# Performance work log

Measured on AMD Instinct MI355X. Metric: run time of the kernel, lower is better.

Reference implementation:

```python
import jax, jax.numpy as jnp
import numpy as np

B, N, D, F, H, C, L = 64, 8192, 5, 16, 4, 4, 4
NEG_SLOPE = 0.2


def setup_inputs() -> dict:
    key = jax.random.key(0)
    ks = jax.random.split(key, 16)
    lin = lambda k, fi, fo: (jax.random.normal(k, (fi, fo), jnp.float32) / np.sqrt(fi)).astype(jnp.float32)
    x = jax.random.normal(ks[0], (B, N, F), jnp.float32)
    agent_nodes = jax.random.randint(ks[1], (B,), 0, N, dtype=jnp.int32)
    neighbors = jax.random.randint(ks[2], (N, D), 0, N, dtype=jnp.int32)
    # GATv2 params (L layers, all 16 -> 4 heads x 4 = 16)
    Wl = jax.random.normal(ks[3], (L, F, H, C), jnp.float32) / np.sqrt(F)
    Wr = jax.random.normal(ks[4], (L, F, H, C), jnp.float32) / np.sqrt(F)
    att_w = jax.random.normal(ks[5], (L, H, C), jnp.float32) / np.sqrt(C)
    bias = jnp.zeros((L, H * C), jnp.float32)
    # global classifier 16->32->64, edge classifier 99->16->8->1
    Wg1, bg1 = lin(ks[6], H * C, 2 * H * C), jnp.zeros(2 * H * C, jnp.float32)
    Wg2, bg2 = lin(ks[7], 2 * H * C, 4 * H * C), jnp.zeros(4 * H * C, jnp.float32)
    e_in = 2 * H * C + 3 + 4 * H * C  # 99
    We1, be1 = lin(ks[8], e_in, H * C), jnp.zeros(H * C, jnp.float32)
    We2, be2 = lin(ks[9], H * C, H * C // 2), jnp.zeros(H * C // 2, jnp.float32)
    We3, be3 = lin(ks[10], H * C // 2, 1), jnp.zeros(1, jnp.float32)
    return dict(x=x, agent_nodes=agent_nodes, neighbors=neighbors, Wl=Wl, Wr=Wr,
                att_w=att_w, bias=bias, Wg1=Wg1, bg1=bg1, Wg2=Wg2, bg2=bg2,
                We1=We1, be1=be1, We2=We2, be2=be2, We3=We3, be3=be3)


def _gatv2_layer(h, src, dst, wl, wr, a, b, n_nodes):
    # h: [B,N,Fin]; wl/wr: [Fin,H,C]; a: [H,C]; b: [H*C]
    xl = jnp.einsum('bnf,fhc->bnhc', h, wl)   # source transform
    xr = jnp.einsum('bnf,fhc->bnhc', h, wr)   # target transform
    hs = xl[:, src]                            # [B,E,H,C]
    ht = xr[:, dst]
    logit = jnp.einsum('behc,hc->beh', jax.nn.leaky_relu(hs + ht, NEG_SLOPE), a)
    lt = logit.transpose(1, 0, 2)              # [E,B,H] (segment ops need E first)
    m = jax.ops.segment_max(lt, dst, num_segments=n_nodes)
    w = jnp.exp(lt - m[dst])
    s = jax.ops.segment_sum(w, dst, num_segments=n_nodes)
    alpha = w / (s[dst] + 1e-16)               # [E,B,H] softmax over in-edges of dst
    msg = alpha[..., None] * hs.transpose(1, 0, 2, 3)
    out = jax.ops.segment_sum(msg, dst, num_segments=n_nodes)  # [N,B,H,C]
    return out.transpose(1, 0, 2, 3).reshape(h.shape[0], n_nodes, -1) + b


def reference(x, agent_nodes, neighbors, Wl, Wr, att_w, bias,
              Wg1, bg1, Wg2, bg2, We1, be1, We2, be2, We3, be3):
    Bn, Nn, _ = x.shape
    Dd = neighbors.shape[1]
    loop = jnp.arange(Nn, dtype=neighbors.dtype)
    src = jnp.concatenate([jnp.repeat(loop, Dd), loop])   # add_self_loops
    dst = jnp.concatenate([neighbors.reshape(-1), loop])
    h = x
    for i in range(Wl.shape[0]):
        h = _gatv2_layer(h, src, dst, Wl[i], Wr[i], att_w[i], bias[i], Nn)
    # global mean aggregation -> 2 SlimFC(tanh)
    agg = jnp.tanh(h.mean(axis=1) @ Wg1 + bg1)
    agg = jnp.tanh(agg @ Wg2 + bg2)                        # [B,64]
    # agent out-edges: source node + its D neighbors
    nb = neighbors[agent_nodes]                            # [B,D]
    bi = jnp.arange(Bn)
    source = h[bi, agent_nodes]                            # [B,16]
    target = h[bi[:, None], nb]                            # [B,D,16]
    tok = jnp.eye(3, dtype=h.dtype)                        # 3 one-hot act tokens
    feats = jnp.concatenate([
        jnp.broadcast_to(source[:, None, None, :], (Bn, 3, Dd, source.shape[-1])),
        jnp.broadcast_to(tok[None, :, None, :], (Bn, 3, Dd, 3)),
        jnp.broadcast_to(target[:, None, :, :], (Bn, 3, Dd, target.shape[-1])),
        jnp.broadcast_to(agg[:, None, None, :], (Bn, 3, Dd, agg.shape[-1])),
    ], axis=-1)                                            # [B,3,D,99]
    e = jnp.tanh(feats @ We1 + be1)
    e = jnp.tanh(e @ We2 + be2)
    e = (e @ We3 + be3)[..., 0]                            # [B,3,D]
    # logits[b, turn*D + move] (convert_multidiscrete_action_to_discrete)
    return e.reshape(Bn, 3 * Dd)
```

## Files before the change

kernel.cpp:

```cpp
#include <hip/hip_runtime.h>
#include <hip/hip_fp16.h>
#include <cmath>

#define NNODES 8192
#define NB 64
#define ND 5
#define MAXDEG 64
#define NBLK_L 2048



__global__ void __launch_bounds__(1024)
k_init(const int* __restrict__ agent, const int* __restrict__ nbr,
       int* __restrict__ cnt, int* __restrict__ slot, int* __restrict__ needed) {
  int t = threadIdx.x;
  for (int v = t; v < NNODES; v += 1024) {
    cnt[v] = 1;
    slot[v*MAXDEG] = v;
    needed[v] = 0;
  }
  __syncthreads();
  if (t < NB) {
    int an = agent[t];
    needed[an] = 1;
    #pragma unroll
    for (int d = 0; d < ND; ++d) needed[nbr[an*ND + d]] = 1;
  }
}


__global__ void __launch_bounds__(256)
k_t0fill(const float* __restrict__ x, const float* __restrict__ Wl0, const float* __restrict__ Wr0,
         __half* __restrict__ xl0, __half* __restrict__ xr0,
         const int* __restrict__ nbr, int* __restrict__ cnt, int* __restrict__ slot) {
  if (blockIdx.x >= NBLK_L) {
    int i = (blockIdx.x - NBLK_L)*256 + threadIdx.x;
    if (i < NNODES*ND) {
      int v = nbr[i];
      int pos = atomicAdd(&cnt[v], 1);
      slot[v*MAXDEG + pos] = i/ND;
    }
    return;
  }
  int gid = blockIdx.x*blockDim.x + threadIdx.x;
  int n = gid >> 6;
  int b = gid & 63;
  const float4* src = (const float4*)(x + (((size_t)b*NNODES + n) << 4));
  float hv[16];
  #pragma unroll
  for (int q = 0; q < 4; ++q) *(float4*)(hv+4*q) = src[q];
  float yl[16], yr[16];
  #pragma unroll
  for (int j = 0; j < 16; ++j) { yl[j] = 0.f; yr[j] = 0.f; }
  #pragma unroll
  for (int f = 0; f < 16; ++f) {
    float hf = hv[f];
    #pragma unroll
    for (int j = 0; j < 16; ++j) {
      yl[j] = fmaf(hf, Wl0[f*16+j], yl[j]);
      yr[j] = fmaf(hf, Wr0[f*16+j], yr[j]);
    }
  }
  size_t idx = ((size_t)n << 10) + (b << 4);
  __half2 lh[8], rh[8];
  #pragma unroll
  for (int j = 0; j < 8; ++j) {
    lh[j] = __floats2half2_rn(yl[2*j], yl[2*j+1]);
    rh[j] = __floats2half2_rn(yr[2*j], yr[2*j+1]);
  }
  float4* ld = (float4*)(xl0 + idx);
  ld[0] = *(float4*)&lh[0]; ld[1] = *(float4*)&lh[4];
  float4* rd = (float4*)(xr0 + idx);
  rd[0] = *(float4*)&rh[0]; rd[1] = *(float4*)&rh[4];
}


template<bool LAST>
__global__ void __launch_bounds__(256)
k_layer(const __half* __restrict__ xlin, const __half* __restrict__ xrin,
        __half* __restrict__ xlout, __half* __restrict__ xrout,
        const float* __restrict__ WlNext, const float* __restrict__ WrNext,
        const float* __restrict__ att, const float* __restrict__ bias,
        const int* __restrict__ cnt, const int* __restrict__ slot,
        const int* __restrict__ needed, __half* __restrict__ h,
        float* __restrict__ meanpart) {
  __shared__ float msm[4096];
  int gid = blockIdx.x*blockDim.x + threadIdx.x;
  int v = gid >> 6;
  int b = gid & 63;
  int w = threadIdx.x >> 6;
  size_t boff = (size_t)(b << 4);

  float xr[16];
  {
    const float4* rp = (const float4*)(xrin + ((size_t)v << 10) + boff);
    float4 r0 = rp[0], r1 = rp[1];
    const __half2* pa = (const __half2*)&r0;
    const __half2* pb = (const __half2*)&r1;
    #pragma unroll
    for (int q = 0; q < 4; ++q) { float2 f = __half22float2(pa[q]); xr[2*q] = f.x; xr[2*q+1] = f.y; }
    #pragma unroll
    for (int q = 0; q < 4; ++q) { float2 f = __half22float2(pb[q]); xr[8+2*q] = f.x; xr[8+2*q+1] = f.y; }
  }
  float aw[16];
  #pragma unroll
  for (int j = 0; j < 16; ++j) aw[j] = att[j];

  float s4[4] = {0.f, 0.f, 0.f, 0.f};
  float acc[16];
  #pragma unroll
  for (int j = 0; j < 16; ++j) acc[j] = 0.f;

  int deg = cnt[v];
  const int* sl = slot + v*MAXDEG;

  auto loadrow = [&](int u, float4& r0, float4& r1) {
    const float4* sp = (const float4*)(xlin + ((size_t)u << 10) + boff);
    r0 = sp[0]; r1 = sp[1];
  };
  auto process = [&](const float4& r0, const float4& r1) {
    float t[16];
    const __half2* pa = (const __half2*)&r0;
    const __half2* pb = (const __half2*)&r1;
    #pragma unroll
    for (int q = 0; q < 4; ++q) { float2 f = __half22float2(pa[q]); t[2*q] = f.x; t[2*q+1] = f.y; }
    #pragma unroll
    for (int q = 0; q < 4; ++q) { float2 f = __half22float2(pb[q]); t[8+2*q] = f.x; t[8+2*q+1] = f.y; }
    #pragma unroll
    for (int hh = 0; hh < 4; ++hh) {
      float lg = 0.f;
      #pragma unroll
      for (int c = 0; c < 4; ++c) {
        float z = t[hh*4+c] + xr[hh*4+c];
        z = (z >= 0.f) ? z : 0.2f*z;
        lg = fmaf(z, aw[hh*4+c], lg);
      }
      float p = __expf(lg);
      s4[hh] += p;
      #pragma unroll
      for (int c = 0; c < 4; ++c) acc[hh*4+c] = fmaf(p, t[hh*4+c], acc[hh*4+c]);
    }
  };

  float4 r00,r01, r10,r11, r20,r21, r30,r31, r40,r41, r50,r51, p0,p1;
  loadrow(sl[0], r00, r01);
  if (deg > 1) loadrow(sl[1], r10, r11);
  if (deg > 2) loadrow(sl[2], r20, r21);
  if (deg > 3) loadrow(sl[3], r30, r31);
  if (deg > 4) loadrow(sl[4], r40, r41);
  if (deg > 5) loadrow(sl[5], r50, r51);
  if (deg > 6) loadrow(sl[6], p0, p1);
  process(r00, r01);
  if (deg > 1) process(r10, r11);
  if (deg > 2) process(r20, r21);
  if (deg > 3) process(r30, r31);
  if (deg > 4) process(r40, r41);
  if (deg > 5) process(r50, r51);
  for (int e = 6; e < deg; ++e) {
    float4 c0 = p0, c1 = p1;
    if (e+1 < deg) loadrow(sl[e+1], p0, p1);
    process(c0, c1);
  }

  float o[16];
  #pragma unroll
  for (int hh = 0; hh < 4; ++hh) {
    float inv = 1.f / s4[hh];
    #pragma unroll
    for (int c = 0; c < 4; ++c) o[hh*4+c] = fmaf(acc[hh*4+c], inv, bias[hh*4+c]);
  }

  if (!LAST) {
    float yl[16], yr[16];
    #pragma unroll
    for (int j = 0; j < 16; ++j) { yl[j] = 0.f; yr[j] = 0.f; }
    #pragma unroll
    for (int f = 0; f < 16; ++f) {
      float of = o[f];
      #pragma unroll
      for (int j = 0; j < 16; ++j) {
        yl[j] = fmaf(of, WlNext[f*16+j], yl[j]);
        yr[j] = fmaf(of, WrNext[f*16+j], yr[j]);
      }
    }
    __half2 lh[8], rh[8];
    #pragma unroll
    for (int j = 0; j < 8; ++j) {
      lh[j] = __floats2half2_rn(yl[2*j], yl[2*j+1]);
      rh[j] = __floats2half2_rn(yr[2*j], yr[2*j+1]);
    }
    size_t idx = ((size_t)v << 10) + boff;
    float4* ld = (float4*)(xlout + idx);
    ld[0] = *(float4*)&lh[0]; ld[1] = *(float4*)&lh[4];
    float4* rd = (float4*)(xrout + idx);
    rd[0] = *(float4*)&rh[0]; rd[1] = *(float4*)&rh[4];
  } else {
    if (needed[v]) {
      __half2 oh[8];
      #pragma unroll
      for (int j = 0; j < 8; ++j) oh[j] = __floats2half2_rn(o[2*j], o[2*j+1]);
      float4* hd = (float4*)(h + ((size_t)v << 10) + boff);
      hd[0] = *(float4*)&oh[0]; hd[1] = *(float4*)&oh[4];
    }
    #pragma unroll
    for (int j = 0; j < 16; ++j) msm[(w << 10) + (b << 4) + j] = o[j];
    __syncthreads();
    for (int i = threadIdx.x; i < 1024; i += 256) {
      float s = msm[i] + msm[1024+i] + msm[2048+i] + msm[3072+i];
      meanpart[(size_t)blockIdx.x*1024 + i] = s;
    }
  }
}


__global__ void __launch_bounds__(256)
k_tail(const __half* __restrict__ h, const int* __restrict__ agent,
       const int* __restrict__ nbr, const float* __restrict__ meanpart,
       const float* __restrict__ Wg1, const float* __restrict__ bg1,
       const float* __restrict__ Wg2, const float* __restrict__ bg2,
       const float* __restrict__ We1, const float* __restrict__ be1,
       const float* __restrict__ We2, const float* __restrict__ be2,
       const float* __restrict__ We3, const float* __restrict__ be3,
       float* __restrict__ out) {
  int b = blockIdx.x;
  int t = threadIdx.x;
  __shared__ float red[256];
  __shared__ float mean[16], g1[32], aggs[64];
  __shared__ float srcv[16];
  __shared__ float tgt[5][16];
  __shared__ float e1s[15][16];
  __shared__ float e2s[15][8];
  int an = agent[b];

  {
    int hc = t & 15, grp = t >> 4;
    float s = 0.f;
    for (int p = grp*128; p < grp*128+128; ++p) s += meanpart[(size_t)p*1024 + b*16 + hc];
    red[t] = s;
    __syncthreads();
    if (t < 16) {
      float m = 0.f;
      for (int g = 0; g < 16; ++g) m += red[g*16 + t];
      mean[t] = m * (1.0f/NNODES);
    }
  }
  if (t >= 64 && t < 80) srcv[t-64] = __half2float(h[((size_t)an << 10) + (b << 4) + (t-64)]);
  if (t >= 96 && t < 176) {
    int d = (t-96)/16, k = (t-96)%16;
    int nn = nbr[an*ND + d];
    tgt[d][k] = __half2float(h[((size_t)nn << 10) + (b << 4) + k]);
  }
  __syncthreads();
  if (t < 32) {
    float a = bg1[t];
    for (int f = 0; f < 16; ++f) a = fmaf(mean[f], Wg1[f*32+t], a);
    g1[t] = tanhf(a);
  }
  __syncthreads();
  if (t < 64) {
    float a = bg2[t];
    for (int f = 0; f < 32; ++f) a = fmaf(g1[f], Wg2[f*64+t], a);
    aggs[t] = tanhf(a);
  }
  __syncthreads();
  if (t < 240) {
    int j = t & 15, td = t >> 4;
    int tk = td/5, d = td%5;
    float a = be1[j];
    for (int k = 0; k < 16; ++k) a = fmaf(srcv[k],  We1[k*16+j],      a);
    a += We1[(16+tk)*16 + j];
    for (int k = 0; k < 16; ++k) a = fmaf(tgt[d][k], We1[(19+k)*16+j], a);
    for (int k = 0; k < 64; ++k) a = fmaf(aggs[k],  We1[(35+k)*16+j], a);
    e1s[td][j] = tanhf(a);
  }
  __syncthreads();
  if (t < 120) {
    int j = t & 7, td = t >> 3;
    float a = be2[j];
    for (int k = 0; k < 16; ++k) a = fmaf(e1s[td][k], We2[k*8+j], a);
    e2s[td][j] = tanhf(a);
  }
  __syncthreads();
  if (t < 15) {
    float a = be3[0];
    for (int k = 0; k < 8; ++k) a = fmaf(e2s[t][k], We3[k], a);
    out[b*15 + t] = a;
  }
}


extern "C" void kernel_launch(void* const* d_in, const int* in_sizes, int n_in,
                              void* d_out, int out_size, void* d_ws, size_t ws_size,
                              hipStream_t stream) {
  const float* x     = (const float*)d_in[0];
  const int*   agent = (const int*)  d_in[1];
  const int*   nbr   = (const int*)  d_in[2];
  const float* Wl    = (const float*)d_in[3];
  const float* Wr    = (const float*)d_in[4];
  const float* att   = (const float*)d_in[5];
  const float* bias  = (const float*)d_in[6];
  const float* Wg1   = (const float*)d_in[7];
  const float* bg1   = (const float*)d_in[8];
  const float* Wg2   = (const float*)d_in[9];
  const float* bg2   = (const float*)d_in[10];
  const float* We1   = (const float*)d_in[11];
  const float* be1   = (const float*)d_in[12];
  const float* We2   = (const float*)d_in[13];
  const float* be2   = (const float*)d_in[14];
  const float* We3   = (const float*)d_in[15];
  const float* be3   = (const float*)d_in[16];
  float* out = (float*)d_out;

  char* ws = (char*)d_ws;
  size_t off = 0;
  auto alloc = [&](size_t bytes) -> void* {
    void* p = ws + off;
    off += (bytes + 255) & ~(size_t)255;
    return p;
  };
  const size_t XBYTES  = (size_t)NNODES*NB*16*sizeof(__half);
  __half* h    = (__half*)alloc(XBYTES);
  __half* xlA  = (__half*)alloc(XBYTES);
  __half* xlB  = (__half*)alloc(XBYTES);
  __half* xrA  = (__half*)alloc(XBYTES);
  __half* xrB  = (__half*)alloc(XBYTES);
  int* cnt     = (int*)alloc(NNODES*sizeof(int));
  int* needed  = (int*)alloc(NNODES*sizeof(int));
  int* slot    = (int*)alloc((size_t)NNODES*MAXDEG*sizeof(int));
  float* meanpart = (float*)alloc((size_t)NBLK_L*1024*sizeof(float));

  k_init<<<1, 1024, 0, stream>>>(agent, nbr, cnt, slot, needed);
  k_t0fill<<<NBLK_L + NNODES*ND/256, 256, 0, stream>>>(x, Wl, Wr, xlA, xrA, nbr, cnt, slot);

  k_layer<false><<<NBLK_L, 256, 0, stream>>>(xlA, xrA, xlB, xrB, Wl + 256, Wr + 256,
                                             att,      bias,      cnt, slot, needed, nullptr, nullptr);
  k_layer<false><<<NBLK_L, 256, 0, stream>>>(xlB, xrB, xlA, xrA, Wl + 512, Wr + 512,
                                             att + 16, bias + 16, cnt, slot, needed, nullptr, nullptr);
  k_layer<false><<<NBLK_L, 256, 0, stream>>>(xlA, xrA, xlB, xrB, Wl + 768, Wr + 768,
                                             att + 32, bias + 32, cnt, slot, needed, nullptr, nullptr);
  k_layer<true ><<<NBLK_L, 256, 0, stream>>>(xlB, xrB, nullptr, nullptr, nullptr, nullptr,
                                             att + 48, bias + 48, cnt, slot, needed, h, meanpart);

  k_tail<<<NB, 256, 0, stream>>>(h, agent, nbr, meanpart,
                                 Wg1, bg1, Wg2, bg2,
                                 We1, be1, We2, be2, We3, be3, out);
}
```

Measured before the change: 245.9 us.

## Split each node-batch across two wavefronts and replace init kernel with memset

Each node's 16-channel feature vector per batch element is now split across two wavefronts (8 channels each), so every lane does one 16-byte gather per neighbor instead of two. The two halves are exchanged through shared memory before the next-layer projection. The layer grid doubles to 4096 blocks, which raises parallelism and memory-level concurrency but adds a __syncthreads and doubles the partial-mean buffer that k_tail must reduce. The separate single-block init kernel is replaced by a memset plus extra blocks in the fill kernel, and the self-loop is handled implicitly rather than stored in the slot table.

Result: slower. 305.4 us (+24.2%).

```diff
diff --git a/kernel.cpp b/kernel.cpp
--- a/kernel.cpp
+++ b/kernel.cpp
@@ -6,39 +6,28 @@
 #define NB 64
 #define ND 5
 #define MAXDEG 64
-#define NBLK_L 2048
-
-
-
-__global__ void __launch_bounds__(1024)
-k_init(const int* __restrict__ agent, const int* __restrict__ nbr,
-       int* __restrict__ cnt, int* __restrict__ slot, int* __restrict__ needed) {
-  int t = threadIdx.x;
-  for (int v = t; v < NNODES; v += 1024) {
-    cnt[v] = 1;
-    slot[v*MAXDEG] = v;
-    needed[v] = 0;
-  }
-  __syncthreads();
-  if (t < NB) {
-    int an = agent[t];
-    needed[an] = 1;
-    #pragma unroll
-    for (int d = 0; d < ND; ++d) needed[nbr[an*ND + d]] = 1;
-  }
-}
+#define NBLK_T0 2048
+#define NBLK_LAY 4096
+
 
 
 __global__ void __launch_bounds__(256)
 k_t0fill(const float* __restrict__ x, const float* __restrict__ Wl0, const float* __restrict__ Wr0,
          __half* __restrict__ xl0, __half* __restrict__ xr0,
-         const int* __restrict__ nbr, int* __restrict__ cnt, int* __restrict__ slot) {
-  if (blockIdx.x >= NBLK_L) {
-    int i = (blockIdx.x - NBLK_L)*256 + threadIdx.x;
-    if (i < NNODES*ND) {
+         const int* __restrict__ agent, const int* __restrict__ nbr,
+         int* __restrict__ cnt, int* __restrict__ slot, int* __restrict__ needed) {
+  if (blockIdx.x >= NBLK_T0) {
+    int eb = blockIdx.x - NBLK_T0;
+    if (eb < 160) {
+      int i = eb*256 + threadIdx.x;
       int v = nbr[i];
       int pos = atomicAdd(&cnt[v], 1);
-      slot[v*MAXDEG + pos] = i/ND;
+      slot[v*MAXDEG + 1 + pos] = i/ND;
+    } else if (threadIdx.x < NB) {
+      int an = agent[threadIdx.x];
+      needed[an] = 1;
+      #pragma unroll
+      for (int d = 0; d < ND; ++d) needed[nbr[an*ND + d]] = 1;
     }
     return;
   }
@@ -74,6 +63,12 @@
   rd[0] = *(float4*)&rh[0]; rd[1] = *(float4*)&rh[4];
 }
 
+
+__device__ __forceinline__ void cvt8(const float4& r, float* t) {
+  const __half2* pa = (const __half2*)&r;
+  #pragma unroll
+  for (int q = 0; q < 4; ++q) { float2 f = __half22float2(pa[q]); t[2*q] = f.x; t[2*q+1] = f.y; }
+}
 
 template<bool LAST>
 __global__ void __launch_bounds__(256)
@@ -84,50 +79,40 @@
         const int* __restrict__ cnt, const int* __restrict__ slot,
         const int* __restrict__ needed, __half* __restrict__ h,
         float* __restrict__ meanpart) {
-  __shared__ float msm[4096];
-  int gid = blockIdx.x*blockDim.x + threadIdx.x;
-  int v = gid >> 6;
-  int b = gid & 63;
-  int w = threadIdx.x >> 6;
-  size_t boff = (size_t)(b << 4);
-
-  float xr[16];
+  __shared__ float smem[2048];
+  int tid = threadIdx.x;
+  int w = tid >> 6, lane = tid & 63;
+  int wv = (blockIdx.x << 2) + w;
+  int v = wv >> 1;
+  int p = wv & 1;
+  int hoff = (lane << 4) + (p << 3);
+
+  float xr[8];
   {
-    const float4* rp = (const float4*)(xrin + ((size_t)v << 10) + boff);
-    float4 r0 = rp[0], r1 = rp[1];
-    const __half2* pa = (const __half2*)&r0;
-    const __half2* pb = (const __half2*)&r1;
-    #pragma unroll
-    for (int q = 0; q < 4; ++q) { float2 f = __half22float2(pa[q]); xr[2*q] = f.x; xr[2*q+1] = f.y; }
-    #pragma unroll
-    for (int q = 0; q < 4; ++q) { float2 f = __half22float2(pb[q]); xr[8+2*q] = f.x; xr[8+2*q+1] = f.y; }
-  }
-  float aw[16];
-  #pragma unroll
-  for (int j = 0; j < 16; ++j) aw[j] = att[j];
-
-  float s4[4] = {0.f, 0.f, 0.f, 0.f};
-  float acc[16];
-  #pragma unroll
-  for (int j = 0; j < 16; ++j) acc[j] = 0.f;
+    float4 r = *(const float4*)(xrin + ((size_t)v << 10) + hoff);
+    cvt8(r, xr);
+  }
+  float aw[8];
+  #pragma unroll
+  for (int j = 0; j < 8; ++j) aw[j] = att[(p<<3)+j];
+
+  float s2[2] = {0.f, 0.f};
+  float acc[8];
+  #pragma unroll
+  for (int j = 0; j < 8; ++j) acc[j] = 0.f;
 
   int deg = cnt[v];
+  int tot = deg + 1;
   const int* sl = slot + v*MAXDEG;
 
-  auto loadrow = [&](int u, float4& r0, float4& r1) {
-    const float4* sp = (const float4*)(xlin + ((size_t)u << 10) + boff);
-    r0 = sp[0]; r1 = sp[1];
+  auto loadrow = [&](int u) -> float4 {
+    return *(const float4*)(xlin + ((size_t)u << 10) + hoff);
   };
-  auto process = [&](const float4& r0, const float4& r1) {
-    float t[16];
-    const __half2* pa = (const __half2*)&r0;
-    const __half2* pb = (const __half2*)&r1;
-    #pragma unroll
-    for (int q = 0; q < 4; ++q) { float2 f = __half22float2(pa[q]); t[2*q] = f.x; t[2*q+1] = f.y; }
-    #pragma unroll
-    for (int q = 0; q < 4; ++q) { float2 f = __half22float2(pb[q]); t[8+2*q] = f.x; t[8+2*q+1] = f.y; }
-    #pragma unroll
-    for (int hh = 0; hh < 4; ++hh) {
+  auto process = [&](const float4& r) {
+    float t[8];
+    cvt8(r, t);
+    #pragma unroll
+    for (int hh = 0; hh < 2; ++hh) {
       float lg = 0.f;
       #pragma unroll
       for (int c = 0; c < 4; ++c) {
@@ -135,78 +120,86 @@
         z = (z >= 0.f) ? z : 0.2f*z;
         lg = fmaf(z, aw[hh*4+c], lg);
       }
-      float p = __expf(lg);
-      s4[hh] += p;
-      #pragma unroll
-      for (int c = 0; c < 4; ++c) acc[hh*4+c] = fmaf(p, t[hh*4+c], acc[hh*4+c]);
+      float pw = __expf(lg);
+      s2[hh] += pw;
+      #pragma unroll
+      for (int c = 0; c < 4; ++c) acc[hh*4+c] = fmaf(pw, t[hh*4+c], acc[hh*4+c]);
     }
   };
 
-  float4 r00,r01, r10,r11, r20,r21, r30,r31, r40,r41, r50,r51, p0,p1;
-  loadrow(sl[0], r00, r01);
-  if (deg > 1) loadrow(sl[1], r10, r11);
-  if (deg > 2) loadrow(sl[2], r20, r21);
-  if (deg > 3) loadrow(sl[3], r30, r31);
-  if (deg > 4) loadrow(sl[4], r40, r41);
-  if (deg > 5) loadrow(sl[5], r50, r51);
-  if (deg > 6) loadrow(sl[6], p0, p1);
-  process(r00, r01);
-  if (deg > 1) process(r10, r11);
-  if (deg > 2) process(r20, r21);
-  if (deg > 3) process(r30, r31);
-  if (deg > 4) process(r40, r41);
-  if (deg > 5) process(r50, r51);
-  for (int e = 6; e < deg; ++e) {
-    float4 c0 = p0, c1 = p1;
-    if (e+1 < deg) loadrow(sl[e+1], p0, p1);
-    process(c0, c1);
-  }
-
-  float o[16];
-  #pragma unroll
-  for (int hh = 0; hh < 4; ++hh) {
-    float inv = 1.f / s4[hh];
-    #pragma unroll
-    for (int c = 0; c < 4; ++c) o[hh*4+c] = fmaf(acc[hh*4+c], inv, bias[hh*4+c]);
+  float4 r0, r1, r2, r3, r4, r5, pn;
+  r0 = loadrow(v);
+  if (tot > 1) r1 = loadrow(sl[1]);
+  if (tot > 2) r2 = loadrow(sl[2]);
+  if (tot > 3) r3 = loadrow(sl[3]);
+  if (tot > 4) r4 = loadrow(sl[4]);
+  if (tot > 5) r5 = loadrow(sl[5]);
+  if (tot > 6) pn = loadrow(sl[6]);
+  process(r0);
+  if (tot > 1) process(r1);
+  if (tot > 2) process(r2);
+  if (tot > 3) process(r3);
+  if (tot > 4) process(r4);
+  if (tot > 5) process(r5);
+  for (int e = 6; e < tot; ++e) {
+    float4 c = pn;
+    if (e+1 < tot) pn = loadrow(sl[e+1]);
+    process(c);
+  }
+
+  float o[8];
+  #pragma unroll
+  for (int hh = 0; hh < 2; ++hh) {
+    float inv = 1.f / s2[hh];
+    #pragma unroll
+    for (int c = 0; c < 4; ++c) o[hh*4+c] = fmaf(acc[hh*4+c], inv, bias[(p<<3)+hh*4+c]);
   }
 
   if (!LAST) {
-    float yl[16], yr[16];
-    #pragma unroll
-    for (int j = 0; j < 16; ++j) { yl[j] = 0.f; yr[j] = 0.f; }
+    #pragma unroll
+    for (int j = 0; j < 8; ++j) smem[(w << 9) + (lane << 3) + j] = o[j];
+    __syncthreads();
+    float of[16];
+    #pragma unroll
+    for (int j = 0; j < 8; ++j) of[(p<<3)+j] = o[j];
+    int sw = w ^ 1, po = p ^ 1;
+    #pragma unroll
+    for (int j = 0; j < 8; ++j) of[(po<<3)+j] = smem[(sw << 9) + (lane << 3) + j];
+    float yl[8], yr[8];
+    #pragma unroll
+    for (int j = 0; j < 8; ++j) { yl[j] = 0.f; yr[j] = 0.f; }
     #pragma unroll
     for (int f = 0; f < 16; ++f) {
-      float of = o[f];
-      #pragma unroll
-      for (int j = 0; j < 16; ++j) {
-        yl[j] = fmaf(of, WlNext[f*16+j], yl[j]);
-        yr[j] = fmaf(of, WrNext[f*16+j], yr[j]);
+      float ofv = of[f];
+      #pragma unroll
+      for (int j = 0; j < 8; ++j) {
+        yl[j] = fmaf(ofv, WlNext[f*16 + (p<<3) + j], yl[j]);
+        yr[j] = fmaf(ofv, WrNext[f*16 + (p<<3) + j], yr[j]);
       }
     }
-    __half2 lh[8], rh[8];
-    #pragma unroll
-    for (int j = 0; j < 8; ++j) {
+    __half2 lh[4], rh[4];
+    #pragma unroll
+    for (int j = 0; j < 4; ++j) {
       lh[j] = __floats2half2_rn(yl[2*j], yl[2*j+1]);
       rh[j] = __floats2half2_rn(yr[2*j], yr[2*j+1]);
     }
-    size_t idx = ((size_t)v << 10) + boff;
-    float4* ld = (float4*)(xlout + idx);
-    ld[0] = *(float4*)&lh[0]; ld[1] = *(float4*)&lh[4];
-    float4* rd = (float4*)(xrout + idx);
-    rd[0] = *(float4*)&rh[0]; rd[1] = *(float4*)&rh[4];
+    size_t idx = ((size_t)v << 10) + hoff;
+    *(float4*)(xlout + idx) = *(float4*)&lh[0];
+    *(float4*)(xrout + idx) = *(float4*)&rh[0];
   } else {
     if (needed[v]) {
-      __half2 oh[8];
-      #pragma unroll
-      for (int j = 0; j < 8; ++j) oh[j] = __floats2half2_rn(o[2*j], o[2*j+1]);
-      float4* hd = (float4*)(h + ((size_t)v << 10) + boff);
-      hd[0] = *(float4*)&oh[0]; hd[1] = *(float4*)&oh[4];
-    }
-    #pragma unroll
-    for (int j = 0; j < 16; ++j) msm[(w << 10) + (b << 4) + j] = o[j];
+      __half2 oh[4];
+      #pragma unroll
+      for (int j = 0; j < 4; ++j) oh[j] = __floats2half2_rn(o[2*j], o[2*j+1]);
+      *(float4*)(h + ((size_t)v << 10) + hoff) = *(float4*)&oh[0];
+    }
+    #pragma unroll
+    for (int j = 0; j < 8; ++j) smem[(w << 9) + (lane << 3) + j] = o[j];
     __syncthreads();
-    for (int i = threadIdx.x; i < 1024; i += 256) {
-      float s = msm[i] + msm[1024+i] + msm[2048+i] + msm[3072+i];
+    for (int i = tid; i < 1024; i += 256) {
+      int b = i >> 4, hc = i & 15;
+      int pp = hc >> 3, j = hc & 7;
+      float s = smem[(pp << 9) + (b << 3) + j] + smem[((2+pp) << 9) + (b << 3) + j];
       meanpart[(size_t)blockIdx.x*1024 + i] = s;
     }
   }
@@ -235,7 +228,7 @@
   {
     int hc = t & 15, grp = t >> 4;
     float s = 0.f;
-    for (int p = grp*128; p < grp*128+128; ++p) s += meanpart[(size_t)p*1024 + b*16 + hc];
+    for (int p = grp*256; p < grp*256+256; ++p) s += meanpart[(size_t)p*1024 + b*16 + hc];
     red[t] = s;
     __syncthreads();
     if (t < 16) {
@@ -318,28 +311,30 @@
     off += (bytes + 255) & ~(size_t)255;
     return p;
   };
-  const size_t XBYTES  = (size_t)NNODES*NB*16*sizeof(__half);
+  const size_t XBYTES = (size_t)NNODES*NB*16*sizeof(__half);
   __half* h    = (__half*)alloc(XBYTES);
   __half* xlA  = (__half*)alloc(XBYTES);
   __half* xlB  = (__half*)alloc(XBYTES);
   __half* xrA  = (__half*)alloc(XBYTES);
   __half* xrB  = (__half*)alloc(XBYTES);
-  int* cnt     = (int*)alloc(NNODES*sizeof(int));
-  int* needed  = (int*)alloc(NNODES*sizeof(int));
-  int* slot    = (int*)alloc((size_t)NNODES*MAXDEG*sizeof(int));
-  float* meanpart = (float*)alloc((size_t)NBLK_L*1024*sizeof(float));
-
-  k_init<<<1, 1024, 0, stream>>>(agent, nbr, cnt, slot, needed);
-  k_t0fill<<<NBLK_L + NNODES*ND/256, 256, 0, stream>>>(x, Wl, Wr, xlA, xrA, nbr, cnt, slot);
-
-  k_layer<false><<<NBLK_L, 256, 0, stream>>>(xlA, xrA, xlB, xrB, Wl + 256, Wr + 256,
-                                             att,      bias,      cnt, slot, needed, nullptr, nullptr);
-  k_layer<false><<<NBLK_L, 256, 0, stream>>>(xlB, xrB, xlA, xrA, Wl + 512, Wr + 512,
-                                             att + 16, bias + 16, cnt, slot, needed, nullptr, nullptr);
-  k_layer<false><<<NBLK_L, 256, 0, stream>>>(xlA, xrA, xlB, xrB, Wl + 768, Wr + 768,
-                                             att + 32, bias + 32, cnt, slot, needed, nullptr, nullptr);
-  k_layer<true ><<<NBLK_L, 256, 0, stream>>>(xlB, xrB, nullptr, nullptr, nullptr, nullptr,
-                                             att + 48, bias + 48, cnt, slot, needed, h, meanpart);
+  int*  slot   = (int*)alloc((size_t)NNODES*MAXDEG*sizeof(int));
+  float* meanpart = (float*)alloc((size_t)NBLK_LAY*1024*sizeof(float));
+  int* cnt    = (int*)alloc(NNODES*sizeof(int));
+  int* needed = (int*)alloc(NNODES*sizeof(int));
+
+  hipMemsetAsync(cnt, 0, NNODES*sizeof(int)*2, stream);
+
+  k_t0fill<<<NBLK_T0 + 161, 256, 0, stream>>>(x, Wl, Wr, xlA, xrA,
+                                              agent, nbr, cnt, slot, needed);
+
+  k_layer<false><<<NBLK_LAY, 256, 0, stream>>>(xlA, xrA, xlB, xrB, Wl + 256, Wr + 256,
+                                               att,      bias,      cnt, slot, needed, nullptr, nullptr);
+  k_layer<false><<<NBLK_LAY, 256, 0, stream>>>(xlB, xrB, xlA, xrA, Wl + 512, Wr + 512,
+                                               att + 16, bias + 16, cnt, slot, needed, nullptr, nullptr);
+  k_layer<false><<<NBLK_LAY, 256, 0, stream>>>(xlA, xrA, xlB, xrB, Wl + 768, Wr + 768,
+                                               att + 32, bias + 32, cnt, slot, needed, nullptr, nullptr);
+  k_layer<true ><<<NBLK_LAY, 256, 0, stream>>>(xlB, xrB, nullptr, nullptr, nullptr, nullptr,
+                                               att + 48, bias + 48, cnt, slot, needed, h, meanpart);
 
   k_tail<<<NB, 256, 0, stream>>>(h, agent, nbr, meanpart,
                                  Wg1, bg1, Wg2, bg2,
```
